# Performance work log

Measured on AMD Instinct MI355X. Metric: run time of the kernel, lower is better.

The kernel has to match this reference:

```python
import jax, jax.numpy as jnp
import numpy as np

B, Ng, A, Eg = 32, 2500, 50, 2000      # graphs, atoms/graph, residues/graph, edges/graph
DIN, EDIM, H1, H2, AF, HG = 64, 16, 64, 64, 95, 128
F1, F2, F3 = 64, 32, 16
K, T = 3, 6                             # ARMA num_stacks, num_layers
N, E = B * Ng, B * Eg


def _glorot(k, shape, fan_in):
    return jax.random.normal(k, shape, jnp.float32) / np.sqrt(fan_in)


def setup_inputs():
    key = jax.random.key(0)
    ks = jax.random.split(key, 24)
    x = jax.random.normal(ks[0], (N, DIN), jnp.float32)
    off = (jnp.arange(B) * Ng)[:, None]
    src = (jax.random.randint(ks[1], (B, Eg), 0, Ng) + off).reshape(-1)
    dst = (jax.random.randint(ks[2], (B, Eg), 0, Ng) + off).reshape(-1)
    edge_index = jnp.stack([src, dst])
    edge_attr = jax.random.normal(ks[3], (E, EDIM), jnp.float32)
    monomer_labels = jnp.tile(jnp.arange(Ng) // (Ng // A), B)  # atom -> residue (0..A-1, per graph)
    aminoacids_features = jax.random.normal(ks[4], (B, A, AF), jnp.float32)
    FIN = H2 + AF  # 159, ARMA input dim
    return {
        'x': x, 'edge_index': edge_index, 'edge_attr': edge_attr,
        'monomer_labels': monomer_labels, 'aminoacids_features': aminoacids_features,
        'w_e1': _glorot(ks[5], (EDIM, DIN * H1), EDIM), 'b_e1': jnp.zeros((DIN * H1,)),
        'root1': _glorot(ks[6], (DIN, H1), DIN), 'bias1': jnp.zeros((H1,)),
        'w_e2': _glorot(ks[7], (EDIM, H1 * H2), EDIM), 'b_e2': jnp.zeros((H1 * H2,)),
        'root2': _glorot(ks[8], (H1, H2), H1), 'bias2': jnp.zeros((H2,)),
        'attn_atom_w': _glorot(ks[9], (H2, 1), H2), 'attn_atom_b': jnp.zeros((1,)),
        'arma_init_w': _glorot(ks[10], (K, FIN, HG), FIN),
        'arma_w': _glorot(ks[11], (T - 1, K, HG, HG), HG),
        'arma_root_w': _glorot(ks[12], (T, K, FIN, HG), FIN),
        'arma_bias': jnp.zeros((T, K, 1, HG)),
        'attn_aa_w': _glorot(ks[13], (HG, 1), HG), 'attn_aa_b': jnp.zeros((1,)),
        'w1': _glorot(ks[14], (HG, F1), HG), 'b1': jnp.zeros((F1,)),
        'w2': _glorot(ks[15], (F1, F2), F1), 'b2': jnp.zeros((F2,)),
        'w3': _glorot(ks[16], (F2, F3), F2), 'b3': jnp.zeros((F3,)),
        'w4': _glorot(ks[17], (F3, 1), F3), 'b4': jnp.zeros((1,)),
    }


def reference(x, edge_index, edge_attr, monomer_labels, aminoacids_features,
              w_e1, b_e1, root1, bias1, w_e2, b_e2, root2, bias2,
              attn_atom_w, attn_atom_b, arma_init_w, arma_w, arma_root_w, arma_bias,
              attn_aa_w, attn_aa_b, w1, b1, w2, b2, w3, b3, w4, b4):
    src, dst = edge_index[0], edge_index[1]

    def nnconv(h, w_e, b_e, root, bias):
        din, dout = root.shape
        W = (edge_attr @ w_e + b_e).reshape(-1, din, dout)      # per-edge weight [E, din, dout]
        msg = jnp.einsum('ei,eio->eo', h[src], W)               # per-edge matvec
        agg = jax.ops.segment_sum(msg, dst, num_segments=N)     # scatter-add at dst
        return agg + h @ root + bias

    h = jax.nn.relu(nnconv(x, w_e1, b_e1, root1, bias1))
    h = jax.nn.relu(nnconv(h, w_e2, b_e2, root2, bias2))

    # AttentionReadoutAtom per graph: softmax over atoms, scatter-sum to residues
    hb = h.reshape(B, Ng, H2)
    attn = jax.nn.softmax(hb @ attn_atom_w + attn_atom_b, axis=1)
    wx = (hb * attn).reshape(-1, H2)
    seg = (monomer_labels.reshape(B, Ng) + jnp.arange(B)[:, None] * A).reshape(-1)
    amino = jax.ops.segment_sum(wx, seg, num_segments=B * A).reshape(B, A, H2)
    xi = jnp.concatenate([amino, aminoacids_features], axis=-1)  # [B, A, H2+95]

    # ARMAConv over directed residue chain i->i+1; gcn_norm w/o self-loops:
    # node 0 has in-degree 0 so edge (0,1) gets norm 0, all others norm 1.
    norm = jnp.concatenate([jnp.zeros(1), jnp.ones(A - 2)])      # [A-1]

    def prop(z):  # z: [B, K, A, F]; out[i+1] = norm_i * z[i]
        shifted = z[..., :-1, :] * norm[:, None]
        return jnp.concatenate([jnp.zeros_like(z[..., :1, :]), shifted], axis=-2)

    out = prop(jnp.einsum('baf,kfg->bkag', xi, arma_init_w))
    out = jax.nn.relu(out + jnp.einsum('baf,kfg->bkag', xi, arma_root_w[0]) + arma_bias[0][None])
    for t in range(1, T):
        out = prop(jnp.einsum('bkaf,kfg->bkag', out, arma_w[t - 1]))
        out = jax.nn.relu(out + jnp.einsum('baf,kfg->bkag', xi, arma_root_w[t]) + arma_bias[t][None])
    g = jax.nn.relu(out.mean(axis=1))  # mean over K stacks -> [B, A, HG]

    # AttentionReadoutAminoAcid: softmax over residues, weighted sum
    a = jax.nn.softmax(g @ attn_aa_w + attn_aa_b, axis=1)
    p = (g * a).sum(axis=1)  # [B, HG]

    # MLP head (dropout is identity in eval mode)
    p = jax.nn.relu(p @ w1 + b1)
    p = jax.nn.relu(p @ w2 + b2)
    p = jax.nn.relu(p @ w3 + b3)
    return (p @ w4 + b4).reshape(-1)
```

## Files before the change

kernel.cpp:

```cpp
#include <hip/hip_runtime.h>

#define N_NODES 80000
#define N_EDGES 64000
#define NB      32
#define NG      2500
#define NA      50
#define EDIM    16
#define FIN     159
#define HG      128
#define RICOLS  2688

typedef __attribute__((ext_vector_type(8))) short bf16x8;
typedef __attribute__((ext_vector_type(4))) float f32x4;

__device__ inline ushort rne_bf16(float f) {
    union { float f; unsigned u; } v; v.f = f;
    const unsigned r = v.u + 0x7fffu + ((v.u >> 16) & 1u);
    return (ushort)(r >> 16);
}
__device__ inline float bf16_to_f32(ushort h) {
    union { unsigned u; float f; } v; v.u = ((unsigned)h) << 16;
    return v.f;
}
__device__ __forceinline__ void gl_lds16(const void* gsrc, void* ldst) {
    __builtin_amdgcn_global_load_lds(
        (const __attribute__((address_space(1))) unsigned int*)gsrc,
        (__attribute__((address_space(3))) unsigned int*)ldst, 16, 0, 0);
}

__global__ __launch_bounds__(256) void prep_w2(const float* __restrict__ we1, const float* __restrict__ be1,
    const float* __restrict__ we2, const float* __restrict__ be2,
    ushort* __restrict__ w1h, ushort* __restrict__ w1l, ushort* __restrict__ w2h, ushort* __restrict__ w2l)
{
    int idx = blockIdx.x * 256 + threadIdx.x;
    const int half = (idx >= 17 * 8 * 64) ? 1 : 0;
    if (half) idx -= 17 * 8 * 64;
    if (idx >= 17 * 8 * 64) return;
    const float* we = half ? we2 : we1;
    const float* be = half ? be2 : be1;
    ushort* Wh = half ? w2h : w1h;
    ushort* Wlo = half ? w2l : w1l;
    const int l = idx & 63;
    const int slot = (idx >> 6) & 7;
    const int j = idx >> 9;
    const int n = slot >> 1, kq = slot & 1;
    const int o = n * 16 + (l & 15);
    const int i0 = kq * 32 + (l >> 4) * 8;
    ushort th[8], tl[8];
#pragma unroll
    for (int t = 0; t < 8; ++t) {
        const int i = i0 + t;
        const float f = (j < 16) ? we[j * 4096 + i * 64 + o] : be[i * 64 + o];
        const ushort hi = rne_bf16(f);
        th[t] = hi;
        tl[t] = rne_bf16(f - bf16_to_f32(hi));
    }
    *(uint4*)(Wh + (size_t)idx * 8) = *(const uint4*)th;
    *(uint4*)(Wlo + (size_t)idx * 8) = *(const uint4*)tl;
}

template<int RELU>
__global__ __launch_bounds__(256) void root_gemm(const float* __restrict__ in,
    const float* __restrict__ w, const float* __restrict__ bias, float* __restrict__ out)
{
    __shared__ float At[64 * 65];
    __shared__ float Wl[64 * 64];
    __shared__ float bl[64];
    const int tid = threadIdx.x;
    const int r0 = blockIdx.x * 64;
    for (int s = tid; s < 4096; s += 256) {
        int r = s >> 6, c = s & 63;
        float v = in[(r0 + r) * 64 + c];
        if (RELU) v = fmaxf(v, 0.f);
        At[c * 65 + r] = v;
    }
    for (int s = tid; s < 4096; s += 256) Wl[s] = w[s];
    if (tid < 64) bl[tid] = bias[tid];
    __syncthreads();
    const int tr = tid >> 4, tc = tid & 15;
    float acc[4][4] = {};
#pragma unroll 8
    for (int i = 0; i < 64; ++i) {
        const float4 a4 = *(const float4*)&At[i * 65 + tr * 4];
        const float4 b4 = *(const float4*)&Wl[i * 64 + tc * 4];
        const float av[4] = {a4.x, a4.y, a4.z, a4.w};
        const float bv[4] = {b4.x, b4.y, b4.z, b4.w};
#pragma unroll
        for (int m = 0; m < 4; ++m)
#pragma unroll
            for (int n = 0; n < 4; ++n) acc[m][n] = fmaf(av[m], bv[n], acc[m][n]);
    }
    const float4 bq = *(const float4*)&bl[tc * 4];
#pragma unroll
    for (int m = 0; m < 4; ++m) {
        float4 o4 = {acc[m][0] + bq.x, acc[m][1] + bq.y, acc[m][2] + bq.z, acc[m][3] + bq.w};
        *(float4*)&out[(r0 + tr * 4 + m) * 64 + tc * 4] = o4;
    }
}

#define TE 128
template<int RELU>
__global__ __launch_bounds__(256) void edge_conv_mfma(const float* __restrict__ h,
    const float* __restrict__ ea, const int* __restrict__ src, const int* __restrict__ dst,
    const ushort* __restrict__ Whi, const ushort* __restrict__ Wlo, float* __restrict__ agg)
{
    __shared__ ushort Bst[2][8192];
    __shared__ float  EAt[17 * 132];
    const int tid = threadIdx.x;
    const int e0 = blockIdx.x * TE;
    const int wv = tid >> 6, l = tid & 63;

#pragma unroll
    for (int i = 0; i < 4; ++i) {
        const int c = wv * 4 + i;
        const ushort* gs = (c < 8) ? (Whi + ((size_t)c * 64 + l) * 8)
                                   : (Wlo + ((size_t)(c - 8) * 64 + l) * 8);
        gl_lds16(gs, (char*)(&Bst[0][0]) + c * 1024);
    }
    for (int s = tid; s < TE * 16; s += 256) {
        const int le = s >> 4, j = s & 15;
        EAt[j * 132 + le] = ea[(size_t)(e0 + le) * 16 + j];
    }
    if (tid < TE) EAt[16 * 132 + tid] = 1.0f;

    bf16x8 ah[2][2], al[2][2];
#pragma unroll
    for (int m = 0; m < 2; ++m) {
        const int erow = wv * 32 + m * 16 + (l & 15);
        const int nd = src[e0 + erow];
        const float4* hp = (const float4*)(h + (size_t)nd * 64);
#pragma unroll
        for (int kq = 0; kq < 2; ++kq) {
            const int q0 = kq * 8 + (l >> 4) * 2;
            const float4 v0 = hp[q0], v1 = hp[q0 + 1];
            const float fv[8] = {v0.x, v0.y, v0.z, v0.w, v1.x, v1.y, v1.z, v1.w};
            ushort th[8], tl[8];
#pragma unroll
            for (int t = 0; t < 8; ++t) {
                const float f = RELU ? fmaxf(fv[t], 0.f) : fv[t];
                th[t] = rne_bf16(f);
                tl[t] = rne_bf16(f - bf16_to_f32(th[t]));
            }
            ah[m][kq] = *(const bf16x8*)th;
            al[m][kq] = *(const bf16x8*)tl;
        }
    }
    __syncthreads();

    f32x4 msg[2][4];
#pragma unroll
    for (int m = 0; m < 2; ++m)
#pragma unroll
        for (int n = 0; n < 4; ++n) msg[m][n] = (f32x4)0.f;

#pragma unroll 1
    for (int j = 0; j < 17; ++j) {
        const int cur = j & 1;
        if (j < 16) {
#pragma unroll
            for (int i = 0; i < 4; ++i) {
                const int c = wv * 4 + i;
                const ushort* gs = (c < 8) ? (Whi + ((size_t)((j + 1) * 8 + c) * 64 + l) * 8)
                                           : (Wlo + ((size_t)((j + 1) * 8 + (c - 8)) * 64 + l) * 8);
                gl_lds16(gs, (char*)(&Bst[cur ^ 1][0]) + c * 1024);
            }
        }
        f32x4 eam[2];
        eam[0] = *(const f32x4*)&EAt[j * 132 + wv * 32 + (l >> 4) * 4];
        eam[1] = *(const f32x4*)&EAt[j * 132 + wv * 32 + 16 + (l >> 4) * 4];
#pragma unroll
        for (int n = 0; n < 4; ++n) {
            const char* bb = (const char*)(&Bst[cur][0]);
            const bf16x8 bh0 = *(const bf16x8*)(bb + ((n * 2 + 0) * 64 + l) * 16);
            const bf16x8 bh1 = *(const bf16x8*)(bb + ((n * 2 + 1) * 64 + l) * 16);
            const bf16x8 bl0 = *(const bf16x8*)(bb + 8192 + ((n * 2 + 0) * 64 + l) * 16);
            const bf16x8 bl1 = *(const bf16x8*)(bb + 8192 + ((n * 2 + 1) * 64 + l) * 16);
#pragma unroll
            for (int m = 0; m < 2; ++m) {
                f32x4 t = __builtin_amdgcn_mfma_f32_16x16x32_bf16(ah[m][0], bh0, (f32x4)0.f, 0, 0, 0);
                t = __builtin_amdgcn_mfma_f32_16x16x32_bf16(ah[m][1], bh1, t, 0, 0, 0);
                t = __builtin_amdgcn_mfma_f32_16x16x32_bf16(ah[m][0], bl0, t, 0, 0, 0);
                t = __builtin_amdgcn_mfma_f32_16x16x32_bf16(ah[m][1], bl1, t, 0, 0, 0);
                t = __builtin_amdgcn_mfma_f32_16x16x32_bf16(al[m][0], bh0, t, 0, 0, 0);
                t = __builtin_amdgcn_mfma_f32_16x16x32_bf16(al[m][1], bh1, t, 0, 0, 0);
                msg[m][n] += eam[m] * t;
            }
        }
        __syncthreads();
    }

#pragma unroll
    for (int m = 0; m < 2; ++m)
#pragma unroll
        for (int r = 0; r < 4; ++r) {
            const int erow = wv * 32 + m * 16 + (l >> 4) * 4 + r;
            const size_t d = (size_t)dst[e0 + erow] * 64;
#pragma unroll
            for (int n = 0; n < 4; ++n)
                atomicAdd(&agg[d + n * 16 + (l & 15)], msg[m][n][r]);
        }
}

__global__ __launch_bounds__(256) void scores_k(const float* __restrict__ h2,
    const float* __restrict__ w, const float* __restrict__ b, float* __restrict__ sc)
{
    __shared__ float wl[64];
    if (threadIdx.x < 64) wl[threadIdx.x] = w[threadIdx.x];
    __syncthreads();
    const int n = blockIdx.x * 256 + threadIdx.x;
    if (n < N_NODES) {
        float acc = b[0];
        const float4* hp = (const float4*)(h2 + (long)n * 64);
#pragma unroll
        for (int q = 0; q < 16; ++q) {
            const float4 v = hp[q];
            acc = fmaf(fmaxf(v.x, 0.f), wl[q * 4 + 0], acc); acc = fmaf(fmaxf(v.y, 0.f), wl[q * 4 + 1], acc);
            acc = fmaf(fmaxf(v.z, 0.f), wl[q * 4 + 2], acc); acc = fmaf(fmaxf(v.w, 0.f), wl[q * 4 + 3], acc);
        }
        sc[n] = acc;
    }
}

__global__ __launch_bounds__(256) void softmax_k(const float* __restrict__ sc, float* __restrict__ attn)
{
    __shared__ float red[256];
    const int g = blockIdx.x, tid = threadIdx.x;
    const float* s = sc + (long)g * NG;
    float m = -1e30f;
    for (int a = tid; a < NG; a += 256) m = fmaxf(m, s[a]);
    red[tid] = m; __syncthreads();
    for (int st = 128; st; st >>= 1) { if (tid < st) red[tid] = fmaxf(red[tid], red[tid + st]); __syncthreads(); }
    const float mx = red[0]; __syncthreads();
    float sum = 0.f;
    for (int a = tid; a < NG; a += 256) sum += expf(s[a] - mx);
    red[tid] = sum; __syncthreads();
    for (int st = 128; st; st >>= 1) { if (tid < st) red[tid] += red[tid + st]; __syncthreads(); }
    const float inv = 1.0f / red[0];
    for (int a = tid; a < NG; a += 256) attn[(long)g * NG + a] = expf(s[a] - mx) * inv;
}

__global__ __launch_bounds__(256) void amino_k(const float* __restrict__ h2,
    const float* __restrict__ attn, const float* __restrict__ aa, float* __restrict__ xi)
{
    const int tid = threadIdx.x;
    const int r = blockIdx.x * 4 + (tid >> 6);
    const int o = tid & 63;
    const int g = r / NA, ar = r % NA;
    const long base = (long)g * NG + ar * 50;
    float acc = 0.f;
#pragma unroll 10
    for (int a = 0; a < 50; ++a) acc = fmaf(attn[base + a], fmaxf(h2[(base + a) * 64 + o], 0.f), acc);
    xi[(long)r * FIN + o] = acc;
    for (int s = tid; s < 4 * 95; s += 256) {
        const int lr = s / 95, f = s % 95;
        const int rr = blockIdx.x * 4 + lr;
        xi[(long)rr * FIN + 64 + f] = aa[(long)rr * 95 + f];
    }
}

__global__ __launch_bounds__(256) void ri_gemm(const float* __restrict__ xi,
    const float* __restrict__ rootw, const float* __restrict__ initw,
    const float* __restrict__ abias, float* __restrict__ RI)
{
    __shared__ float At[32 * 65];
    __shared__ float Bl[32 * 64];
    const int tid = threadIdx.x;
    const int r0 = blockIdx.x * 64, c0 = blockIdx.y * 64;
    const int blk = c0 >> 7;
    const int gb = c0 & 127;
    const float* bsrc = (blk < 18) ? (rootw + (long)blk * FIN * 128) : (initw + (long)(blk - 18) * FIN * 128);
    const int tr = tid >> 4, tc = tid & 15;
    float acc[4][4] = {};
    for (int f0 = 0; f0 < FIN; f0 += 32) {
        __syncthreads();
        for (int s = tid; s < 64 * 32; s += 256) {
            const int r = s >> 5, kk = s & 31; const int f = f0 + kk;
            At[kk * 65 + r] = (f < FIN) ? xi[(long)(r0 + r) * FIN + f] : 0.f;
        }
        for (int s = tid; s < 32 * 64; s += 256) {
            const int kk = s >> 6, cc = s & 63; const int f = f0 + kk;
            Bl[s] = (f < FIN) ? bsrc[(long)f * 128 + gb + cc] : 0.f;
        }
        __syncthreads();
#pragma unroll 8
        for (int kk = 0; kk < 32; ++kk) {
            const float4 a4 = *(const float4*)&At[kk * 65 + tr * 4];
            const float4 b4 = *(const float4*)&Bl[kk * 64 + tc * 4];
            const float av[4] = {a4.x, a4.y, a4.z, a4.w};
            const float bv[4] = {b4.x, b4.y, b4.z, b4.w};
#pragma unroll
            for (int m = 0; m < 4; ++m)
#pragma unroll
                for (int n = 0; n < 4; ++n) acc[m][n] = fmaf(av[m], bv[n], acc[m][n]);
        }
    }
    float4 bq = {0.f, 0.f, 0.f, 0.f};
    if (blk < 18) bq = *(const float4*)&abias[c0 + tc * 4];
#pragma unroll
    for (int m = 0; m < 4; ++m) {
        float4 o4 = {acc[m][0] + bq.x, acc[m][1] + bq.y, acc[m][2] + bq.z, acc[m][3] + bq.w};
        *(float4*)&RI[(long)(r0 + tr * 4 + m) * RICOLS + c0 + tc * 4] = o4;
    }
}

__global__ __launch_bounds__(256) void arma_all(const float* __restrict__ RI,
    const float* __restrict__ armaw, float* __restrict__ G)
{
    __shared__ float X[2][32 * 128];
    __shared__ float Wl[128 * 128];
    const int bid = blockIdx.x;
    const int g = bid / 6, k = (bid % 6) >> 1, half = bid & 1;
    const int tid = threadIdx.x;
    const int r0 = half ? 20 : 0;
    const size_t rbase = (size_t)g * NA;

    for (int s = tid; s < 30 * 128; s += 256) {
        const int a = r0 + (s >> 7), o = s & 127;
        float v = RI[(rbase + a) * RICOLS + k * 128 + o];
        if (a >= 2) v += RI[(rbase + a - 1) * RICOLS + (18 + k) * 128 + o];
        X[0][s] = fmaxf(v, 0.f);
    }
    int cur = 0;
    const int rg = tid >> 5;
    const int cg = tid & 31;
    for (int t = 1; t <= 5; ++t) {
        __syncthreads();
        const float* W = armaw + (size_t)((t - 1) * 3 + k) * 16384;
        for (int s = tid; s < 4096; s += 256) ((float4*)Wl)[s] = ((const float4*)W)[s];
        __syncthreads();
        float acc[4][4] = {};
#pragma unroll 4
        for (int f0 = 0; f0 < 128; f0 += 4) {
            float4 wv[4];
#pragma unroll
            for (int i = 0; i < 4; ++i) wv[i] = *(const float4*)&Wl[(f0 + i) * 128 + cg * 4];
#pragma unroll
            for (int m = 0; m < 4; ++m) {
                const int lr = rg * 4 + m;
                const int pl = (lr >= 1) ? lr - 1 : 0;
                const float4 xv = *(const float4*)&X[cur][pl * 128 + f0];
#pragma unroll
                for (int n = 0; n < 4; ++n) {
                    acc[m][n] = fmaf(xv.x, ((const float*)&wv[0])[n], acc[m][n]);
                    acc[m][n] = fmaf(xv.y, ((const float*)&wv[1])[n], acc[m][n]);
                    acc[m][n] = fmaf(xv.z, ((const float*)&wv[2])[n], acc[m][n]);
                    acc[m][n] = fmaf(xv.w, ((const float*)&wv[3])[n], acc[m][n]);
                }
            }
        }
        __syncthreads();
#pragma unroll
        for (int m = 0; m < 4; ++m) {
            const int lr = rg * 4 + m;
            if (lr < 30) {
                const int a = r0 + lr;
                const bool prop = (a >= 2) && (lr >= 1);
                const float4 rv = *(const float4*)&RI[(rbase + a) * RICOLS + (t * 3 + k) * 128 + cg * 4];
                float4 ov;
                ov.x = fmaxf((prop ? acc[m][0] : 0.f) + rv.x, 0.f);
                ov.y = fmaxf((prop ? acc[m][1] : 0.f) + rv.y, 0.f);
                ov.z = fmaxf((prop ? acc[m][2] : 0.f) + rv.z, 0.f);
                ov.w = fmaxf((prop ? acc[m][3] : 0.f) + rv.w, 0.f);
                *(float4*)&X[cur ^ 1][lr * 128 + cg * 4] = ov;
            }
        }
        cur ^= 1;
    }
    __syncthreads();
    const int w0 = half ? 25 : 0;
    for (int s = tid; s < 25 * 128; s += 256) {
        const int a = w0 + (s >> 7), o = s & 127;
        G[((size_t)k * 1600 + rbase + a) * 128 + o] = X[cur][(a - r0) * 128 + o];
    }
}

__global__ __launch_bounds__(256) void final_k(const float* __restrict__ G,
    const float* __restrict__ waa, const float* __restrict__ baa,
    const float* __restrict__ w1, const float* __restrict__ b1,
    const float* __restrict__ w2, const float* __restrict__ b2,
    const float* __restrict__ w3, const float* __restrict__ b3,
    const float* __restrict__ w4, const float* __restrict__ b4, float* __restrict__ out)
{
    __shared__ float gl[50 * 129];
    __shared__ float sc[64];
    __shared__ float pl[128];
    __shared__ float h1l[64], h2l[32], h3l[16];
    __shared__ float wl[128];
    const int b = blockIdx.x, tid = threadIdx.x;
    for (int s = tid; s < 50 * 128; s += 256) {
        const int a = s >> 7, o = s & 127;
        const size_t r = ((size_t)b * 50 + a) * 128 + o;
        const float v = (G[r] + G[(size_t)1600 * 128 + r] + G[(size_t)2 * 1600 * 128 + r]) * (1.f / 3.f);
        gl[a * 129 + o] = fmaxf(v, 0.f);
    }
    if (tid < 128) wl[tid] = waa[tid];
    __syncthreads();
    if (tid < 50) {
        float acc = baa[0];
        for (int f = 0; f < 128; ++f) acc = fmaf(gl[tid * 129 + f], wl[f], acc);
        sc[tid] = acc;
    }
    __syncthreads();
    if (tid < 64) {
        const float v = (tid < 50) ? sc[tid] : -1e30f;
        float m = v;
        for (int d = 32; d; d >>= 1) m = fmaxf(m, __shfl_xor(m, d));
        const float e = (tid < 50) ? expf(v - m) : 0.f;
        float ssum = e;
        for (int d = 32; d; d >>= 1) ssum += __shfl_xor(ssum, d);
        if (tid < 50) sc[tid] = e / ssum;
    }
    __syncthreads();
    if (tid < 128) {
        float acc = 0.f;
        for (int a = 0; a < 50; ++a) acc = fmaf(sc[a], gl[a * 129 + tid], acc);
        pl[tid] = acc;
    }
    __syncthreads();
    if (tid < 64) {
        float acc = b1[tid];
        for (int f = 0; f < 128; ++f) acc = fmaf(pl[f], w1[f * 64 + tid], acc);
        h1l[tid] = fmaxf(acc, 0.f);
    }
    __syncthreads();
    if (tid < 32) {
        float acc = b2[tid];
        for (int f = 0; f < 64; ++f) acc = fmaf(h1l[f], w2[f * 32 + tid], acc);
        h2l[tid] = fmaxf(acc, 0.f);
    }
    __syncthreads();
    if (tid < 16) {
        float acc = b3[tid];
        for (int f = 0; f < 32; ++f) acc = fmaf(h2l[f], w3[f * 16 + tid], acc);
        h3l[tid] = fmaxf(acc, 0.f);
    }
    __syncthreads();
    if (tid == 0) {
        float acc = b4[0];
        for (int f = 0; f < 16; ++f) acc = fmaf(h3l[f], w4[f], acc);
        out[b] = acc;
    }
}

extern "C" void kernel_launch(void* const* d_in, const int* in_sizes, int n_in,
                              void* d_out, int out_size, void* d_ws, size_t ws_size,
                              hipStream_t stream) {
    const float* x     = (const float*)d_in[0];
    const int*   eidx  = (const int*)d_in[1];
    const float* ea    = (const float*)d_in[2];
    const float* aaf   = (const float*)d_in[4];
    const float* we1   = (const float*)d_in[5];
    const float* be1   = (const float*)d_in[6];
    const float* root1 = (const float*)d_in[7];
    const float* bias1 = (const float*)d_in[8];
    const float* we2   = (const float*)d_in[9];
    const float* be2   = (const float*)d_in[10];
    const float* root2 = (const float*)d_in[11];
    const float* bias2 = (const float*)d_in[12];
    const float* waw   = (const float*)d_in[13];
    const float* wab   = (const float*)d_in[14];
    const float* initw = (const float*)d_in[15];
    const float* armaw = (const float*)d_in[16];
    const float* rootw = (const float*)d_in[17];
    const float* abias = (const float*)d_in[18];
    const float* waa   = (const float*)d_in[19];
    const float* baa   = (const float*)d_in[20];
    const float* w1    = (const float*)d_in[21];
    const float* b1    = (const float*)d_in[22];
    const float* w2    = (const float*)d_in[23];
    const float* b2    = (const float*)d_in[24];
    const float* w3    = (const float*)d_in[25];
    const float* b3    = (const float*)d_in[26];
    const float* w4    = (const float*)d_in[27];
    const float* b4    = (const float*)d_in[28];
    float* out = (float*)d_out;

    const int* src = eidx;
    const int* dst = eidx + N_EDGES;

    char* ws = (char*)d_ws;
    size_t off = 0;
    float* h1     = (float*)(ws + off); off += (size_t)N_NODES * 64 * 4;
    float* h2     = (float*)(ws + off); off += (size_t)N_NODES * 64 * 4;
    float* scores = (float*)(ws + off); off += (size_t)N_NODES * 4;
    float* attn   = (float*)(ws + off); off += (size_t)N_NODES * 4;
    float* xi     = (float*)(ws + off); off += (size_t)1600 * FIN * 4;
    float* RI     = (float*)(ws + off); off += (size_t)1600 * RICOLS * 4;
    float* G      = (float*)(ws + off); off += (size_t)3 * 1600 * 128 * 4;
    ushort* wt1h  = (ushort*)(ws + off); off += (size_t)17 * 8 * 64 * 8 * 2;
    ushort* wt1l  = (ushort*)(ws + off); off += (size_t)17 * 8 * 64 * 8 * 2;
    ushort* wt2h  = (ushort*)(ws + off); off += (size_t)17 * 8 * 64 * 8 * 2;
    ushort* wt2l  = (ushort*)(ws + off); off += (size_t)17 * 8 * 64 * 8 * 2;

    prep_w2<<<68, 256, 0, stream>>>(we1, be1, we2, be2, wt1h, wt1l, wt2h, wt2l);

    root_gemm<0><<<N_NODES / 64, 256, 0, stream>>>(x, root1, bias1, h1);
    edge_conv_mfma<0><<<N_EDGES / TE, 256, 0, stream>>>(x, ea, src, dst, wt1h, wt1l, h1);
    root_gemm<1><<<N_NODES / 64, 256, 0, stream>>>(h1, root2, bias2, h2);
    edge_conv_mfma<1><<<N_EDGES / TE, 256, 0, stream>>>(h1, ea, src, dst, wt2h, wt2l, h2);
    scores_k<<<(N_NODES + 255) / 256, 256, 0, stream>>>(h2, waw, wab, scores);
    softmax_k<<<NB, 256, 0, stream>>>(scores, attn);
    amino_k<<<1600 / 4, 256, 0, stream>>>(h2, attn, aaf, xi);
    ri_gemm<<<dim3(25, 42), 256, 0, stream>>>(xi, rootw, initw, abias, RI);
    arma_all<<<NB * 6, 256, 0, stream>>>(RI, armaw, G);
    final_k<<<NB, 256, 0, stream>>>(G, waa, baa, w1, b1, w2, b2, w3, b3, w4, b4, out);
}
```

Measured before the change: 347.9 us.

## Run ARMA recurrence on bf16x3 MFMA with pre-swizzled split weights

Moves the ARMA stack recurrence from scalar FP32 FMAs to 16x16x32 bf16 MFMA. Both operands are split into hi/lo bf16 parts (three MFMAs per tile) to keep near-FP32 accuracy. A new prep kernel pre-swizzles the ARMA weights into the MFMA fragment layout, and those fragments are now read straight from global memory instead of being staged into LDS. The block shrinks to 128 threads (two waves) and the X buffer gets padded rows, which lowers occupancy per block but removes the per-step weight staging syncs. It also adds one extra small kernel launch.

```diff
diff --git a/kernel.cpp b/kernel.cpp
--- a/kernel.cpp
+++ b/kernel.cpp
@@ -9,6 +9,7 @@
 #define FIN     159
 #define HG      128
 #define RICOLS  2688
+#define XSTR    132
 
 typedef __attribute__((ext_vector_type(8))) short bf16x8;
 typedef __attribute__((ext_vector_type(4))) float f32x4;
@@ -59,6 +60,29 @@
     *(uint4*)(Wlo + (size_t)idx * 8) = *(const uint4*)tl;
 }
 
+__global__ __launch_bounds__(256) void prep_arma(const float* __restrict__ armaw,
+    ushort* __restrict__ Bh, ushort* __restrict__ Bl)
+{
+    const int idx = blockIdx.x * 256 + threadIdx.x;
+    if (idx >= 15 * 32 * 64) return;
+    const int l = idx & 63;
+    const int slot = (idx >> 6) & 31;
+    const int ws = idx >> 11;
+    const int n = slot >> 2, kt = slot & 3;
+    const int c = n * 16 + (l & 15);
+    const int f0 = kt * 32 + (l >> 4) * 8;
+    ushort th[8], tl[8];
+#pragma unroll
+    for (int t = 0; t < 8; ++t) {
+        const float v = armaw[(size_t)ws * 16384 + (size_t)(f0 + t) * 128 + c];
+        const ushort hi = rne_bf16(v);
+        th[t] = hi;
+        tl[t] = rne_bf16(v - bf16_to_f32(hi));
+    }
+    *(uint4*)(Bh + (size_t)idx * 8) = *(const uint4*)th;
+    *(uint4*)(Bl + (size_t)idx * 8) = *(const uint4*)tl;
+}
+
 template<int RELU>
 __global__ __launch_bounds__(256) void root_gemm(const float* __restrict__ in,
     const float* __restrict__ w, const float* __restrict__ bias, float* __restrict__ out)
@@ -303,74 +327,84 @@
     }
 }
 
-__global__ __launch_bounds__(256) void arma_all(const float* __restrict__ RI,
-    const float* __restrict__ armaw, float* __restrict__ G)
-{
-    __shared__ float X[2][32 * 128];
-    __shared__ float Wl[128 * 128];
+__global__ __launch_bounds__(128) void arma_all(const float* __restrict__ RI,
+    const ushort* __restrict__ Bh, const ushort* __restrict__ Bl, float* __restrict__ G)
+{
+    __shared__ float Xl[2][32 * XSTR];
     const int bid = blockIdx.x;
     const int g = bid / 6, k = (bid % 6) >> 1, half = bid & 1;
     const int tid = threadIdx.x;
     const int r0 = half ? 20 : 0;
     const size_t rbase = (size_t)g * NA;
 
-    for (int s = tid; s < 30 * 128; s += 256) {
-        const int a = r0 + (s >> 7), o = s & 127;
+    for (int s = tid; s < 30 * 128; s += 128) {
+        const int lr = s >> 7, o = s & 127;
+        const int a = r0 + lr;
         float v = RI[(rbase + a) * RICOLS + k * 128 + o];
         if (a >= 2) v += RI[(rbase + a - 1) * RICOLS + (18 + k) * 128 + o];
-        X[0][s] = fmaxf(v, 0.f);
-    }
+        Xl[0][lr * XSTR + o] = fmaxf(v, 0.f);
+    }
+    for (int s = tid; s < 2 * 128; s += 128) {
+        const int lr = 30 + (s >> 7), o = s & 127;
+        Xl[0][lr * XSTR + o] = 0.f;
+        Xl[1][lr * XSTR + o] = 0.f;
+    }
+
+    const int wv = tid >> 6, l = tid & 63;
+    const int arow = wv * 16 + (l & 15);
+    const bool avalid = (arow >= 1) && (r0 + arow >= 2);
+    const int asrc = avalid ? (arow - 1) : 0;
     int cur = 0;
-    const int rg = tid >> 5;
-    const int cg = tid & 31;
+
     for (int t = 1; t <= 5; ++t) {
         __syncthreads();
-        const float* W = armaw + (size_t)((t - 1) * 3 + k) * 16384;
-        for (int s = tid; s < 4096; s += 256) ((float4*)Wl)[s] = ((const float4*)W)[s];
-        __syncthreads();
-        float acc[4][4] = {};
-#pragma unroll 4
-        for (int f0 = 0; f0 < 128; f0 += 4) {
-            float4 wv[4];
-#pragma unroll
-            for (int i = 0; i < 4; ++i) wv[i] = *(const float4*)&Wl[(f0 + i) * 128 + cg * 4];
-#pragma unroll
-            for (int m = 0; m < 4; ++m) {
-                const int lr = rg * 4 + m;
-                const int pl = (lr >= 1) ? lr - 1 : 0;
-                const float4 xv = *(const float4*)&X[cur][pl * 128 + f0];
-#pragma unroll
-                for (int n = 0; n < 4; ++n) {
-                    acc[m][n] = fmaf(xv.x, ((const float*)&wv[0])[n], acc[m][n]);
-                    acc[m][n] = fmaf(xv.y, ((const float*)&wv[1])[n], acc[m][n]);
-                    acc[m][n] = fmaf(xv.z, ((const float*)&wv[2])[n], acc[m][n]);
-                    acc[m][n] = fmaf(xv.w, ((const float*)&wv[3])[n], acc[m][n]);
+        bf16x8 ah[4], al[4];
+#pragma unroll
+        for (int kt = 0; kt < 4; ++kt) {
+            const float* xp = &Xl[cur][asrc * XSTR + kt * 32 + (l >> 4) * 8];
+            const float4 v0 = *(const float4*)xp;
+            const float4 v1 = *(const float4*)(xp + 4);
+            const float fv[8] = {v0.x, v0.y, v0.z, v0.w, v1.x, v1.y, v1.z, v1.w};
+            ushort th[8], tl[8];
+#pragma unroll
+            for (int t8 = 0; t8 < 8; ++t8) {
+                const float f = avalid ? fv[t8] : 0.f;
+                th[t8] = rne_bf16(f);
+                tl[t8] = rne_bf16(f - bf16_to_f32(th[t8]));
+            }
+            ah[kt] = *(const bf16x8*)th;
+            al[kt] = *(const bf16x8*)tl;
+        }
+        const size_t wsbase = (size_t)(((t - 1) * 3 + k) * 32) * 64 * 8;
+#pragma unroll
+        for (int n = 0; n < 8; ++n) {
+            f32x4 acc = (f32x4)0.f;
+#pragma unroll
+            for (int kt = 0; kt < 4; ++kt) {
+                const size_t fo = wsbase + (size_t)(n * 4 + kt) * 64 * 8 + (size_t)l * 8;
+                const bf16x8 bh = *(const bf16x8*)(Bh + fo);
+                const bf16x8 bl8 = *(const bf16x8*)(Bl + fo);
+                acc = __builtin_amdgcn_mfma_f32_16x16x32_bf16(ah[kt], bh, acc, 0, 0, 0);
+                acc = __builtin_amdgcn_mfma_f32_16x16x32_bf16(ah[kt], bl8, acc, 0, 0, 0);
+                acc = __builtin_amdgcn_mfma_f32_16x16x32_bf16(al[kt], bh, acc, 0, 0, 0);
+            }
+            const int cn = n * 16 + (l & 15);
+#pragma unroll
+            for (int r = 0; r < 4; ++r) {
+                const int lr = wv * 16 + (l >> 4) * 4 + r;
+                if (lr < 30) {
+                    const float rv = RI[(rbase + r0 + lr) * RICOLS + (t * 3 + k) * 128 + cn];
+                    Xl[cur ^ 1][lr * XSTR + cn] = fmaxf(acc[r] + rv, 0.f);
                 }
             }
         }
-        __syncthreads();
-#pragma unroll
-        for (int m = 0; m < 4; ++m) {
-            const int lr = rg * 4 + m;
-            if (lr < 30) {
-                const int a = r0 + lr;
-                const bool prop = (a >= 2) && (lr >= 1);
-                const float4 rv = *(const float4*)&RI[(rbase + a) * RICOLS + (t * 3 + k) * 128 + cg * 4];
-                float4 ov;
-                ov.x = fmaxf((prop ? acc[m][0] : 0.f) + rv.x, 0.f);
-                ov.y = fmaxf((prop ? acc[m][1] : 0.f) + rv.y, 0.f);
-                ov.z = fmaxf((prop ? acc[m][2] : 0.f) + rv.z, 0.f);
-                ov.w = fmaxf((prop ? acc[m][3] : 0.f) + rv.w, 0.f);
-                *(float4*)&X[cur ^ 1][lr * 128 + cg * 4] = ov;
-            }
-        }
         cur ^= 1;
     }
     __syncthreads();
     const int w0 = half ? 25 : 0;
-    for (int s = tid; s < 25 * 128; s += 256) {
+    for (int s = tid; s < 25 * 128; s += 128) {
         const int a = w0 + (s >> 7), o = s & 127;
-        G[((size_t)k * 1600 + rbase + a) * 128 + o] = X[cur][(a - r0) * 128 + o];
+        G[((size_t)k * 1600 + rbase + a) * 128 + o] = Xl[cur][(a - r0) * XSTR + o];
     }
 }
 
@@ -491,8 +525,11 @@
     ushort* wt1l  = (ushort*)(ws + off); off += (size_t)17 * 8 * 64 * 8 * 2;
     ushort* wt2h  = (ushort*)(ws + off); off += (size_t)17 * 8 * 64 * 8 * 2;
     ushort* wt2l  = (ushort*)(ws + off); off += (size_t)17 * 8 * 64 * 8 * 2;
+    ushort* abh   = (ushort*)(ws + off); off += (size_t)15 * 32 * 64 * 8 * 2;
+    ushort* abl   = (ushort*)(ws + off); off += (size_t)15 * 32 * 64 * 8 * 2;
 
     prep_w2<<<68, 256, 0, stream>>>(we1, be1, we2, be2, wt1h, wt1l, wt2h, wt2l);
+    prep_arma<<<120, 256, 0, stream>>>(armaw, abh, abl);
 
     root_gemm<0><<<N_NODES / 64, 256, 0, stream>>>(x, root1, bias1, h1);
     edge_conv_mfma<0><<<N_EDGES / TE, 256, 0, stream>>>(x, ea, src, dst, wt1h, wt1l, h1);
@@ -502,6 +539,6 @@
     softmax_k<<<NB, 256, 0, stream>>>(scores, attn);
     amino_k<<<1600 / 4, 256, 0, stream>>>(h2, attn, aaf, xi);
     ri_gemm<<<dim3(25, 42), 256, 0, stream>>>(xi, rootw, initw, abias, RI);
-    arma_all<<<NB * 6, 256, 0, stream>>>(RI, armaw, G);
+    arma_all<<<NB * 6, 128, 0, stream>>>(RI, abh, abl, G);
     final_k<<<NB, 256, 0, stream>>>(G, waa, baa, w1, b1, w2, b2, w3, b3, w4, b4, out);
 }
```

After: 386.8 us. 11.2% more time.
